# Kernel optimization log

Measured on AMD Instinct MI355X. Metric: run time of the kernel, lower is better.

Reference implementation:

```python
import jax, jax.numpy as jnp
import numpy as np

B, F, T, EPT, S, E, H, LVL = 16384, 512, 4, 2, 2, 256, 128, 2

def _ple_level(xs_task, x_sh, w_task, b_task, w_sh, b_sh, w_gate, b_gate, w_gsh=None, b_gsh=None):
    # xs_task: [T,B,I] per-task inputs; x_sh: [B,I] shared input
    task_out = jax.nn.relu(jnp.einsum('tbi,teio->tbeo', xs_task, w_task) + b_task[:, None])  # [T,B,EPT,E]
    sh_out = jax.nn.relu(jnp.einsum('bi,sio->bso', x_sh, w_sh) + b_sh)                       # [B,S,E]
    t = task_out.shape[0]
    experts = jnp.concatenate([task_out, jnp.broadcast_to(sh_out[None], (t,) + sh_out.shape)], axis=2)  # [T,B,EPT+S,E]
    gate = jax.nn.softmax(jnp.einsum('tbi,tig->tbg', xs_task, w_gate) + b_gate[:, None], axis=-1)
    task_next = jnp.einsum('tbg,tbge->tbe', gate, experts)  # [T,B,E]
    sh_next = None
    if w_gsh is not None:
        # all experts ordered task0_exp0, task0_exp1, task1_exp0, ..., then shared
        bsz = x_sh.shape[0]
        all_exp = jnp.concatenate([jnp.transpose(task_out, (1, 0, 2, 3)).reshape(bsz, -1, task_out.shape[-1]), sh_out], axis=1)
        gsh = jax.nn.softmax(x_sh @ w_gsh + b_gsh, axis=-1)
        sh_next = jnp.einsum('bg,bge->be', gsh, all_exp)
    return task_next, sh_next

def setup_inputs() -> dict:
    key = jax.random.key(0)
    ks = jax.random.split(key, 16)
    sc = 0.02
    d = {
        'x': jax.random.normal(ks[0], (B, F), jnp.float32),
        # level 0 (in_dim=F, has shared gate)
        'w_task0': jax.random.normal(ks[1], (T, EPT, F, E), jnp.float32) * sc,
        'b_task0': jnp.zeros((T, EPT, E), jnp.float32),
        'w_sh0': jax.random.normal(ks[2], (S, F, E), jnp.float32) * sc,
        'b_sh0': jnp.zeros((S, E), jnp.float32),
        'w_gate0': jax.random.normal(ks[3], (T, F, EPT + S), jnp.float32) * sc,
        'b_gate0': jnp.zeros((T, EPT + S), jnp.float32),
        'w_gsh0': jax.random.normal(ks[4], (F, T * EPT + S), jnp.float32) * sc,
        'b_gsh0': jnp.zeros((T * EPT + S,), jnp.float32),
        # level 1 (last; in_dim=E, no shared gate)
        'w_task1': jax.random.normal(ks[5], (T, EPT, E, E), jnp.float32) * sc,
        'b_task1': jnp.zeros((T, EPT, E), jnp.float32),
        'w_sh1': jax.random.normal(ks[6], (S, E, E), jnp.float32) * sc,
        'b_sh1': jnp.zeros((S, E), jnp.float32),
        'w_gate1': jax.random.normal(ks[7], (T, E, EPT + S), jnp.float32) * sc,
        'b_gate1': jnp.zeros((T, EPT + S), jnp.float32),
        # towers
        'w_tw': jax.random.normal(ks[8], (T, E, H), jnp.float32) * sc,
        'b_tw': jnp.zeros((T, H), jnp.float32),
        'w_out': jax.random.normal(ks[9], (T, H, 2), jnp.float32) * sc,
        'b_out': jnp.zeros((T, 2), jnp.float32),
    }
    return d

def reference(x, w_task0, b_task0, w_sh0, b_sh0, w_gate0, b_gate0, w_gsh0, b_gsh0,
              w_task1, b_task1, w_sh1, b_sh1, w_gate1, b_gate1,
              w_tw, b_tw, w_out, b_out):
    xs_task = jnp.broadcast_to(x[None], (T,) + x.shape)  # all tasks see same input at level 0
    t1, sh1 = _ple_level(xs_task, x, w_task0, b_task0, w_sh0, b_sh0, w_gate0, b_gate0, w_gsh0, b_gsh0)
    t2, _ = _ple_level(t1, sh1, w_task1, b_task1, w_sh1, b_sh1, w_gate1, b_gate1)
    h = jax.nn.relu(jnp.einsum('tbe,teh->tbh', t2, w_tw) + b_tw[:, None])
    logits = jnp.einsum('tbh,tho->tbo', h, w_out) + b_out[:, None]
    p = jax.nn.softmax(logits, axis=-1)
    return jnp.clip(p, 1e-15, 1.0 - 1e-15)  # [T,B,2]
```

## Files before the change

### kernel.cpp

```cpp
#include <hip/hip_runtime.h>

typedef unsigned short u16;
typedef __bf16 bf16x8 __attribute__((ext_vector_type(8)));
typedef float f32x4 __attribute__((ext_vector_type(4)));
typedef u16 u16x8 __attribute__((ext_vector_type(8)));

#define B_ 16384

__device__ __forceinline__ u16 f2b(float f){
  unsigned u = __builtin_bit_cast(unsigned, f);
  u = (u + 0x7FFFu + ((u >> 16) & 1u)) >> 16;
  return (u16)u;
}
__device__ __forceinline__ float b2f(u16 v){
  return __builtin_bit_cast(float, ((unsigned)v) << 16);
}
__device__ __forceinline__ void ld8(const u16* __restrict__ p, float* f){
  u16x8 v = *(const u16x8*)p;
  #pragma unroll
  for (int j = 0; j < 8; ++j) f[j] = b2f(v[j]);
}
__device__ __forceinline__ void st8(u16* __restrict__ p, const float* f){
  u16x8 v;
  #pragma unroll
  for (int j = 0; j < 8; ++j) v[j] = f2b(f[j]);
  *(u16x8*)p = v;
}

__device__ __forceinline__ void gload16(const u16* g, u16* lds){
  __builtin_amdgcn_global_load_lds(
      (const __attribute__((address_space(1))) unsigned int*)g,
      (__attribute__((address_space(3))) unsigned int*)lds, 16, 0, 0);
}

__device__ __forceinline__ void core32(const u16* __restrict__ A,
                                       const u16* __restrict__ Wt,
                                       int K, int m0, int n0, int nt,
                                       u16* sm, f32x4 acc[4][4])
{
  const int tid = threadIdx.x, lane = tid & 63, wave = tid >> 6;
  const int wm = ((tid >> 7) & 3) * 64;
  const int wn = ((tid >> 6) & 1) * 64;

  #pragma unroll
  for (int m = 0; m < 4; ++m)
    #pragma unroll
    for (int n = 0; n < 4; ++n) acc[m][n] = (f32x4){0.f, 0.f, 0.f, 0.f};

  const int s_    = (lane & 7) ^ ((lane >> 3) & 7);
  const int srow2 = 2 * (lane >> 3) + (s_ >> 2);
  const int sk    = (s_ & 3) * 8;
  const u16* gsrc[3];
  int gdst[3];
  #pragma unroll
  for (int i = 0; i < 3; ++i) {
    int c = wave * 3 + i;
    if (c < 16) {
      gsrc[i] = A + (size_t)(m0 + c * 16 + srow2) * K + sk;
      gdst[i] = c * 512;
    } else {
      gsrc[i] = Wt + (size_t)(n0 + (c - 16) * 16 + srow2) * K + sk;
      gdst[i] = 8192 + (c - 16) * 512;
    }
  }

  int aoff[4], boff[4];
  #pragma unroll
  for (int m = 0; m < 4; ++m) {
    int r = wm + m * 16 + (lane & 15);
    int L = r >> 1;
    int phys = (((r & 1) << 2) + (lane >> 4)) ^ (L & 7);
    aoff[m] = L * 64 + phys * 8;
  }
  #pragma unroll
  for (int n = 0; n < 4; ++n) {
    int r = wn + n * 16 + (lane & 15);
    int L = r >> 1;
    int phys = (((r & 1) << 2) + (lane >> 4)) ^ (L & 7);
    boff[n] = 8192 + L * 64 + phys * 8;
  }

  #pragma unroll
  for (int j = 0; j < 2; ++j) {
    u16* sl = sm + j * 12288;
    #pragma unroll
    for (int i = 0; i < 3; ++i) gload16(gsrc[i] + j * 32, sl + gdst[i]);
  }
  asm volatile("s_waitcnt vmcnt(3)" ::: "memory");
  __builtin_amdgcn_s_barrier();

  int cs = 0;
  for (int j = 0; j < nt; ++j) {
    if (j + 2 < nt) {
      int ns = cs + 2; ns = (ns >= 3) ? ns - 3 : ns;
      u16* sl = sm + ns * 12288;
      #pragma unroll
      for (int i = 0; i < 3; ++i) gload16(gsrc[i] + (size_t)(j + 2) * 32, sl + gdst[i]);
    }
    const u16* sa = sm + cs * 12288;
    bf16x8 av[4], bv[4];
    #pragma unroll
    for (int m = 0; m < 4; ++m) av[m] = *(const bf16x8*)(sa + aoff[m]);
    #pragma unroll
    for (int n = 0; n < 4; ++n) bv[n] = *(const bf16x8*)(sa + boff[n]);
    __builtin_amdgcn_s_setprio(1);
    #pragma unroll
    for (int m = 0; m < 4; ++m)
      #pragma unroll
      for (int n = 0; n < 4; ++n)
        acc[m][n] = __builtin_amdgcn_mfma_f32_16x16x32_bf16(av[m], bv[n], acc[m][n], 0, 0, 0);
    __builtin_amdgcn_s_setprio(0);
    if (j + 2 < nt)      asm volatile("s_waitcnt vmcnt(3)" ::: "memory");
    else if (j + 1 < nt) asm volatile("s_waitcnt vmcnt(0)" ::: "memory");
    __builtin_amdgcn_s_barrier();
    cs = (cs == 2) ? 0 : cs + 1;
  }
}


__global__ __launch_bounds__(512) void k_gemm0(const u16* __restrict__ xb,
    const u16* __restrict__ Wt0, const float* __restrict__ bias0,
    u16* __restrict__ E0, float* __restrict__ G0L)
{
  __shared__ __align__(16) u16 sm[36864];
  f32x4 acc[4][4];
  const int bid = blockIdx.x;
  const int swz = (bid & 7) * 168 + (bid >> 3);
  const int m0 = (swz / 21) * 256, n0 = (swz % 21) * 128;
  core32(xb, Wt0, 512, m0, n0, 16, sm, acc);
  const int lane = threadIdx.x & 63;
  const int wm = ((threadIdx.x >> 7) & 3) * 64, wn = ((threadIdx.x >> 6) & 1) * 64;
  #pragma unroll
  for (int mi = 0; mi < 4; ++mi)
    #pragma unroll
    for (int ni = 0; ni < 4; ++ni) {
      int gcol = n0 + wn + ni * 16 + (lane & 15);
      float bias = bias0[gcol];
      #pragma unroll
      for (int q = 0; q < 4; ++q) {
        int grow = m0 + wm + mi * 16 + ((lane >> 4) << 2) + q;
        float v = acc[mi][ni][q] + bias;
        if (gcol < 2560)      E0[(size_t)grow * 2560 + gcol] = f2b(fmaxf(v, 0.f));
        else if (gcol < 2586) G0L[(size_t)grow * 26 + (gcol - 2560)] = v;
      }
    }
}

__global__ __launch_bounds__(256) void k_mix0(const u16* __restrict__ E0,
    const float* __restrict__ G0L, const float* __restrict__ WG1T,
    const float* __restrict__ b_gate1, u16* __restrict__ T1SH,
    float* __restrict__ G1S)
{
  const int b = blockIdx.x * 8 + (threadIdx.x >> 5);
  const int e0 = (threadIdx.x & 31) * 8;
  const float* gl = G0L + (size_t)b * 26;
  float g[4][4];
  #pragma unroll
  for (int t = 0; t < 4; ++t) {
    float l0 = gl[t*4+0], l1 = gl[t*4+1], l2 = gl[t*4+2], l3 = gl[t*4+3];
    float m = fmaxf(fmaxf(l0, l1), fmaxf(l2, l3));
    float e0e = expf(l0-m), e1 = expf(l1-m), e2 = expf(l2-m), e3 = expf(l3-m);
    float inv = 1.f / (e0e + e1 + e2 + e3);
    g[t][0] = e0e*inv; g[t][1] = e1*inv; g[t][2] = e2*inv; g[t][3] = e3*inv;
  }
  float gs[10];
  {
    float m = gl[16];
    #pragma unroll
    for (int j = 1; j < 10; ++j) m = fmaxf(m, gl[16 + j]);
    float s = 0.f;
    #pragma unroll
    for (int j = 0; j < 10; ++j) { gs[j] = expf(gl[16 + j] - m); s += gs[j]; }
    float inv = 1.f / s;
    #pragma unroll
    for (int j = 0; j < 10; ++j) gs[j] *= inv;
  }
  const u16* row = E0 + (size_t)b * 2560;
  float sh0[8], sh1[8], shacc[8];
  ld8(row + 2048 + e0, sh0);
  ld8(row + 2304 + e0, sh1);
  #pragma unroll
  for (int j = 0; j < 8; ++j) shacc[j] = gs[8]*sh0[j] + gs[9]*sh1[j];
  float gp[16];
  #pragma unroll
  for (int t = 0; t < 4; ++t) {
    float te0[8], te1[8], v[8];
    ld8(row + (t*2+0)*256 + e0, te0);
    ld8(row + (t*2+1)*256 + e0, te1);
    #pragma unroll
    for (int j = 0; j < 8; ++j) {
      v[j] = g[t][0]*te0[j] + g[t][1]*te1[j] + g[t][2]*sh0[j] + g[t][3]*sh1[j];
      shacc[j] += gs[t*2+0]*te0[j] + gs[t*2+1]*te1[j];
    }
    st8(T1SH + ((size_t)t * B_ + b) * 256 + e0, v);
    #pragma unroll
    for (int gg = 0; gg < 4; ++gg) {
      const float* wv = WG1T + ((size_t)(t * 4 + gg) * 256 + e0);
      float s = 0.f;
      #pragma unroll
      for (int j = 0; j < 8; ++j) s += v[j] * wv[j];
      gp[t * 4 + gg] = s;
    }
  }
  st8(T1SH + ((size_t)4 * B_ + b) * 256 + e0, shacc);
  #pragma unroll
  for (int i = 0; i < 16; ++i) {
    #pragma unroll
    for (int off = 1; off < 32; off <<= 1)
      gp[i] += __shfl_xor(gp[i], off, 32);
  }
  if ((threadIdx.x & 31) == 0) {
    float* orow = G1S + (size_t)b * 16;
    #pragma unroll
    for (int z = 0; z < 4; ++z) {
      float l0 = gp[z*4+0] + b_gate1[z*4+0];
      float l1 = gp[z*4+1] + b_gate1[z*4+1];
      float l2 = gp[z*4+2] + b_gate1[z*4+2];
      float l3 = gp[z*4+3] + b_gate1[z*4+3];
      float m = fmaxf(fmaxf(l0, l1), fmaxf(l2, l3));
      float x0 = expf(l0-m), x1 = expf(l1-m), x2 = expf(l2-m), x3 = expf(l3-m);
      float inv = 1.f / (x0 + x1 + x2 + x3);
      orow[z*4+0] = x0*inv; orow[z*4+1] = x1*inv;
      orow[z*4+2] = x2*inv; orow[z*4+3] = x3*inv;
    }
  }
}

__global__ __launch_bounds__(512) void k_gemm1(const u16* __restrict__ T1SH,
    const u16* __restrict__ Wt1, const float* __restrict__ bias1,
    u16* __restrict__ E1, u16* __restrict__ SH1E)
{
  __shared__ __align__(16) u16 sm[36864];
  f32x4 acc[4][4];
  const int bid = blockIdx.x;
  const int swz = (bid & 7) * 160 + (bid >> 3);
  const int mi_ = swz / 20, pan = swz % 20;
  const int z  = pan >> 2;
  const int n0 = (pan & 3) * 128;
  const int m0 = mi_ * 256;
  core32(T1SH + (size_t)z * B_ * 256, Wt1 + (size_t)z * 512 * 256, 256, m0, n0, 8, sm, acc);
  const int lane = threadIdx.x & 63;
  const int wm = ((threadIdx.x >> 7) & 3) * 64, wn = ((threadIdx.x >> 6) & 1) * 64;
  const float* bias = bias1 + z * 512;
  #pragma unroll
  for (int mi = 0; mi < 4; ++mi)
    #pragma unroll
    for (int ni = 0; ni < 4; ++ni) {
      int gcol = n0 + wn + ni * 16 + (lane & 15);
      float bv = bias[gcol];
      #pragma unroll
      for (int q = 0; q < 4; ++q) {
        int grow = m0 + wm + mi * 16 + ((lane >> 4) << 2) + q;
        float v = fmaxf(acc[mi][ni][q] + bv, 0.f);
        if (z < 4) E1[((size_t)z * B_ + grow) * 512 + gcol] = f2b(v);
        else       SH1E[(size_t)grow * 512 + gcol] = f2b(v);
      }
    }
}

__global__ __launch_bounds__(256) void k_tower2(const u16* __restrict__ E1,
    const u16* __restrict__ SH1E, const float* __restrict__ G1S,
    const u16* __restrict__ Wtw, const float* __restrict__ b_tw,
    const float* __restrict__ w_out, const float* __restrict__ b_out,
    float* __restrict__ out)
{
  __shared__ __align__(16) u16 sm[32768];
  __shared__ float part[2][128][2];
  f32x4 acc[4][4];
  const int z = blockIdx.z;
  const int m0 = blockIdx.x * 128;
  const int tid = threadIdx.x, lane = tid & 63, wave = tid >> 6;
  const int wm = ((tid >> 7) & 1) * 64, wn = ((tid >> 6) & 1) * 64;

  #pragma unroll
  for (int mi = 0; mi < 4; ++mi)
    #pragma unroll
    for (int ni = 0; ni < 4; ++ni) acc[mi][ni] = (f32x4){0.f, 0.f, 0.f, 0.f};

  const int srow  = lane >> 3;
  const int gslot = (lane & 7) ^ srow;
  const int koff0 = gslot * 8;

  int growA[4], adst[4], bdst[4];
  const u16* bsrc[4];
  #pragma unroll
  for (int i = 0; i < 4; ++i) {
    int c = wave * 4 + i;
    growA[i] = m0 + c * 8 + srow;
    adst[i]  = c * 512;
    bsrc[i]  = Wtw + (size_t)z * 128 * 256 + (size_t)(c * 8 + srow) * 256 + koff0;
    bdst[i]  = 8192 + c * 512;
  }
  const u16* E1z = E1 + (size_t)z * B_ * 512;

  int aoff[2][4], boff[2][4];
  #pragma unroll
  for (int kk = 0; kk < 2; ++kk) {
    #pragma unroll
    for (int m = 0; m < 4; ++m) {
      int r = wm + m * 16 + (lane & 15);
      aoff[kk][m] = r * 64 + (((kk * 4 + (lane >> 4)) ^ (r & 7)) * 8);
    }
    #pragma unroll
    for (int n = 0; n < 4; ++n) {
      int r = wn + n * 16 + (lane & 15);
      boff[kk][n] = 8192 + r * 64 + (((kk * 4 + (lane >> 4)) ^ (r & 7)) * 8);
    }
  }

  #define STAGE_T(J, BUF) do {                                                 \
    u16* buf_ = (BUF);                                                         \
    _Pragma("unroll")                                                          \
    for (int i_ = 0; i_ < 4; ++i_) {                                           \
      size_t eoff_ = (size_t)growA[i_] * 512 + (J) * 64 + koff0;               \
      u16x8 ea_ = *(const u16x8*)(E1z + eoff_);                                \
      u16x8 eb_ = *(const u16x8*)(E1z + eoff_ + 256);                          \
      u16x8 sa_ = *(const u16x8*)(SH1E + eoff_);                               \
      u16x8 sb_ = *(const u16x8*)(SH1E + eoff_ + 256);                         \
      float4 g_ = *(const float4*)(G1S + (size_t)growA[i_] * 16 + z * 4);      \
      u16x8 o_;                                                                \
      _Pragma("unroll")                                                        \
      for (int jj_ = 0; jj_ < 8; ++jj_)                                        \
        o_[jj_] = f2b(g_.x * b2f(ea_[jj_]) + g_.y * b2f(eb_[jj_])              \
                    + g_.z * b2f(sa_[jj_]) + g_.w * b2f(sb_[jj_]));            \
      *(uint4*)(buf_ + adst[i_] + lane * 8) = __builtin_bit_cast(uint4, o_);   \
      gload16(bsrc[i_] + (J) * 64, buf_ + bdst[i_]);                           \
    }                                                                          \
  } while (0)

  STAGE_T(0, sm);
  __syncthreads();

  #pragma unroll
  for (int t = 0; t < 4; ++t) {
    if (t + 1 < 4) STAGE_T(t + 1, sm + ((t + 1) & 1) * 16384);
    const u16* sa = sm + (t & 1) * 16384;
    #pragma unroll
    for (int kk = 0; kk < 2; ++kk) {
      bf16x8 av[4], bv[4];
      #pragma unroll
      for (int m = 0; m < 4; ++m) av[m] = *(const bf16x8*)(sa + aoff[kk][m]);
      #pragma unroll
      for (int n = 0; n < 4; ++n) bv[n] = *(const bf16x8*)(sa + boff[kk][n]);
      #pragma unroll
      for (int m = 0; m < 4; ++m)
        #pragma unroll
        for (int n = 0; n < 4; ++n)
          acc[m][n] = __builtin_amdgcn_mfma_f32_16x16x32_bf16(av[m], bv[n], acc[m][n], 0, 0, 0);
    }
    if (t + 1 < 4) __syncthreads();
  }
  #undef STAGE_T

  #pragma unroll
  for (int mi = 0; mi < 4; ++mi) {
    #pragma unroll
    for (int r = 0; r < 4; ++r) {
      float p0 = 0.f, p1 = 0.f;
      #pragma unroll
      for (int ni = 0; ni < 4; ++ni) {
        int col = wn + ni * 16 + (lane & 15);
        float h = fmaxf(acc[mi][ni][r] + b_tw[z * 128 + col], 0.f);
        p0 += h * w_out[(z * 128 + col) * 2 + 0];
        p1 += h * w_out[(z * 128 + col) * 2 + 1];
      }
      #pragma unroll
      for (int off = 1; off < 16; off <<= 1) {
        p0 += __shfl_xor(p0, off);
        p1 += __shfl_xor(p1, off);
      }
      if ((lane & 15) == 0) {
        int rowl = wm + mi * 16 + ((lane >> 4) << 2) + r;
        part[wn >> 6][rowl][0] = p0;
        part[wn >> 6][rowl][1] = p1;
      }
    }
  }
  __syncthreads();
  if (threadIdx.x < 128) {
    int rowl = threadIdx.x;
    float l0 = part[0][rowl][0] + part[1][rowl][0] + b_out[z * 2 + 0];
    float l1 = part[0][rowl][1] + part[1][rowl][1] + b_out[z * 2 + 1];
    float mx = fmaxf(l0, l1);
    float e0 = expf(l0 - mx), e1 = expf(l1 - mx);
    float inv = 1.f / (e0 + e1);
    float p0 = fminf(fmaxf(e0 * inv, 1e-15f), 1.0f);
    float p1 = fminf(fmaxf(e1 * inv, 1e-15f), 1.0f);
    size_t o = ((size_t)z * B_ + m0 + rowl) * 2;
    out[o] = p0; out[o + 1] = p1;
  }
}

__global__ void k_prep(const float* __restrict__ x,
    const float* __restrict__ w_task0, const float* __restrict__ b_task0,
    const float* __restrict__ w_sh0,   const float* __restrict__ b_sh0,
    const float* __restrict__ w_gate0, const float* __restrict__ b_gate0,
    const float* __restrict__ w_gsh0,  const float* __restrict__ b_gsh0,
    const float* __restrict__ w_task1, const float* __restrict__ b_task1,
    const float* __restrict__ w_sh1,   const float* __restrict__ b_sh1,
    const float* __restrict__ w_gate1, const float* __restrict__ w_tw,
    u16* __restrict__ xb, u16* __restrict__ Wt0, float* __restrict__ bias0,
    u16* __restrict__ Wt1, float* __restrict__ bias1, u16* __restrict__ Wtw,
    float* __restrict__ WG1T)
{
  size_t i = (size_t)blockIdx.x * 256 + threadIdx.x;
  const size_t S_X8  = (size_t)16384 * 512 / 8;
  const size_t S_WT0 = (size_t)2816 * 512;
  const size_t S_B0  = 2816;
  const size_t S_WT1 = (size_t)5 * 512 * 256;
  const size_t S_B1  = 5 * 512;
  const size_t S_WTW = (size_t)4 * 128 * 256;
  const size_t S_WG1 = 4096;

  if (i < S_X8) {
    size_t o = i * 8;
    float4 a = *(const float4*)(x + o);
    float4 b = *(const float4*)(x + o + 4);
    u16x8 v;
    v[0] = f2b(a.x); v[1] = f2b(a.y); v[2] = f2b(a.z); v[3] = f2b(a.w);
    v[4] = f2b(b.x); v[5] = f2b(b.y); v[6] = f2b(b.z); v[7] = f2b(b.w);
    *(u16x8*)(xb + o) = v;
    return;
  }
  i -= S_X8;
  if (i < S_WT0) {
    int c = (int)(i / 512), f = (int)(i % 512);
    float v = 0.f;
    if (c < 2048)      { int te = c >> 8, o = c & 255; v = w_task0[((size_t)te * 512 + f) * 256 + o]; }
    else if (c < 2560) { int s = (c - 2048) >> 8, o = c & 255; v = w_sh0[((size_t)s * 512 + f) * 256 + o]; }
    else if (c < 2576) { int q = c - 2560; int t = q >> 2, gg = q & 3; v = w_gate0[((size_t)t * 512 + f) * 4 + gg]; }
    else if (c < 2586) { int j = c - 2576; v = w_gsh0[(size_t)f * 10 + j]; }
    Wt0[i] = f2b(v);
    return;
  }
  i -= S_WT0;
  if (i < S_B0) {
    int c = (int)i; float v = 0.f;
    if (c < 2048)      { int te = c >> 8, o = c & 255; v = b_task0[te * 256 + o]; }
    else if (c < 2560) { int s = (c - 2048) >> 8, o = c & 255; v = b_sh0[s * 256 + o]; }
    else if (c < 2576) { v = b_gate0[c - 2560]; }
    else if (c < 2586) { v = b_gsh0[c - 2576]; }
    bias0[c] = v;
    return;
  }
  i -= S_B0;
  if (i < S_WT1) {
    int z = (int)(i / (512 * 256)); int rem = (int)(i % (512 * 256));
    int c = rem / 256, f = rem % 256;
    float v;
    if (z < 4) { int ee = c >> 8, o = c & 255; v = w_task1[(((size_t)(z * 2 + ee)) * 256 + f) * 256 + o]; }
    else       { int s = c >> 8, o = c & 255; v = w_sh1[((size_t)s * 256 + f) * 256 + o]; }
    Wt1[i] = f2b(v);
    return;
  }
  i -= S_WT1;
  if (i < S_B1) {
    int z = (int)(i / 512); int c = (int)(i % 512);
    float v;
    if (z < 4) { int ee = c >> 8, o = c & 255; v = b_task1[(z * 2 + ee) * 256 + o]; }
    else       { int s = c >> 8, o = c & 255; v = b_sh1[s * 256 + o]; }
    bias1[(size_t)z * 512 + c] = v;
    return;
  }
  i -= S_B1;
  if (i < S_WTW) {
    int z = (int)(i / (128 * 256)); int rem = (int)(i % (128 * 256));
    int h = rem / 256, f = rem % 256;
    Wtw[i] = f2b(w_tw[((size_t)z * 256 + f) * 128 + h]);
    return;
  }
  i -= S_WTW;
  if (i < S_WG1) {
    int t = (int)(i >> 10), gg = (int)((i >> 8) & 3), e = (int)(i & 255);
    WG1T[i] = w_gate1[((size_t)t * 256 + e) * 4 + gg];
    return;
  }
}

extern "C" void kernel_launch(void* const* d_in, const int* in_sizes, int n_in,
                              void* d_out, int out_size, void* d_ws, size_t ws_size,
                              hipStream_t stream)
{
  (void)in_sizes; (void)n_in; (void)out_size; (void)ws_size;
  const float* x       = (const float*)d_in[0];
  const float* w_task0 = (const float*)d_in[1];
  const float* b_task0 = (const float*)d_in[2];
  const float* w_sh0   = (const float*)d_in[3];
  const float* b_sh0   = (const float*)d_in[4];
  const float* w_gate0 = (const float*)d_in[5];
  const float* b_gate0 = (const float*)d_in[6];
  const float* w_gsh0  = (const float*)d_in[7];
  const float* b_gsh0  = (const float*)d_in[8];
  const float* w_task1 = (const float*)d_in[9];
  const float* b_task1 = (const float*)d_in[10];
  const float* w_sh1   = (const float*)d_in[11];
  const float* b_sh1   = (const float*)d_in[12];
  const float* w_gate1 = (const float*)d_in[13];
  const float* b_gate1 = (const float*)d_in[14];
  const float* w_tw    = (const float*)d_in[15];
  const float* b_tw    = (const float*)d_in[16];
  const float* w_out   = (const float*)d_in[17];
  const float* b_out   = (const float*)d_in[18];
  float* out = (float*)d_out;

  char* ws = (char*)d_ws;
  u16*   XB    = (u16*)  (ws + 0);
  u16*   SH1E  = (u16*)  (ws + 0);
  u16*   WT0   = (u16*)  (ws + 16777216);
  float* BIAS0 = (float*)(ws + 19660800);
  u16*   WT1   = (u16*)  (ws + 19672064);
  float* BIAS1 = (float*)(ws + 20982784);
  u16*   WTW   = (u16*)  (ws + 20993024);
  u16*   E0    = (u16*)  (ws + 21255168);
  float* G0L   = (float*)(ws + 105141248);
  u16*   T1SH  = (u16*)  (ws + 106845184);
  u16*   E1    = (u16*)  (ws + 148788224);
  float* G1S   = (float*)(ws + 215897088);
  float* WG1T  = (float*)(ws + 216945664);

  k_prep<<<12837, 256, 0, stream>>>(x, w_task0, b_task0, w_sh0, b_sh0, w_gate0, b_gate0,
      w_gsh0, b_gsh0, w_task1, b_task1, w_sh1, b_sh1, w_gate1, w_tw,
      XB, WT0, BIAS0, WT1, BIAS1, WTW, WG1T);
  k_gemm0<<<1344, 512, 0, stream>>>(XB, WT0, BIAS0, E0, G0L);
  k_mix0<<<2048, 256, 0, stream>>>(E0, G0L, WG1T, b_gate1, T1SH, G1S);
  k_gemm1<<<1280, 512, 0, stream>>>(T1SH, WT1, BIAS1, E1, SH1E);
  k_tower2<<<dim3(128, 1, 4), 256, 0, stream>>>(E1, SH1E, G1S, WTW, b_tw, w_out, b_out, out);
}
```

Baseline: 172.0 us.

## Fuse level-0 expert gating into task GEMM epilogue, split gate and shared GEMMs

Level 0 is split into three kernels. A small kernel computes the gate logits and softmaxes. A GEMM produces the shared experts. A task-expert GEMM, whose weights are interleaved so that each 128-column tile holds all 8 task experts for 16 output features, applies the gated mixing in its epilogue through LDS and writes T1SH directly. This removes the large E0 intermediate (B×2560 bf16) round trip and the separate mix pass, at the cost of extra kernel launches, a serial gate kernel that uses wave reductions, and scattered 2-byte SH0E reads in the epilogue.

```diff
diff --git a/kernel.cpp b/kernel.cpp
--- a/kernel.cpp
+++ b/kernel.cpp
@@ -4,6 +4,7 @@
 typedef __bf16 bf16x8 __attribute__((ext_vector_type(8)));
 typedef float f32x4 __attribute__((ext_vector_type(4)));
 typedef u16 u16x8 __attribute__((ext_vector_type(8)));
+typedef u16 u16x4 __attribute__((ext_vector_type(4)));
 
 #define B_ 16384
 
@@ -118,16 +119,72 @@
 }
 
 
-__global__ __launch_bounds__(512) void k_gemm0(const u16* __restrict__ xb,
-    const u16* __restrict__ Wt0, const float* __restrict__ bias0,
-    u16* __restrict__ E0, float* __restrict__ G0L)
+__global__ __launch_bounds__(256) void k_gate0(const u16* __restrict__ xb,
+    const u16* __restrict__ WG0T, const float* __restrict__ b_gate0,
+    const float* __restrict__ b_gsh0, float* __restrict__ G0S)
+{
+  const int lane = threadIdx.x & 63, wave = threadIdx.x >> 6;
+  const int rbase = blockIdx.x * 64 + wave * 16;
+  u16x8 w[26];
+  #pragma unroll
+  for (int g = 0; g < 26; ++g)
+    w[g] = *(const u16x8*)(WG0T + (size_t)g * 512 + lane * 8);
+  float bias[26];
+  #pragma unroll
+  for (int g = 0; g < 26; ++g) bias[g] = (g < 16) ? b_gate0[g] : b_gsh0[g - 16];
+
+  for (int it = 0; it < 16; ++it) {
+    int row = rbase + it;
+    float f[8]; ld8(xb + (size_t)row * 512 + lane * 8, f);
+    float lg[26];
+    #pragma unroll
+    for (int g = 0; g < 26; ++g) {
+      float p = 0.f;
+      #pragma unroll
+      for (int j = 0; j < 8; ++j) p += f[j] * b2f(w[g][j]);
+      #pragma unroll
+      for (int off = 1; off < 64; off <<= 1) p += __shfl_xor(p, off);
+      lg[g] = p + bias[g];
+    }
+    float tg[16];
+    #pragma unroll
+    for (int t = 0; t < 4; ++t) {
+      float m = fmaxf(fmaxf(lg[4*t], lg[4*t+1]), fmaxf(lg[4*t+2], lg[4*t+3]));
+      float e0 = expf(lg[4*t]-m), e1 = expf(lg[4*t+1]-m);
+      float e2 = expf(lg[4*t+2]-m), e3 = expf(lg[4*t+3]-m);
+      float inv = 1.f / (e0+e1+e2+e3);
+      tg[4*t] = e0*inv; tg[4*t+1] = e1*inv; tg[4*t+2] = e2*inv; tg[4*t+3] = e3*inv;
+    }
+    float sg[10];
+    {
+      float m = lg[16];
+      #pragma unroll
+      for (int j = 1; j < 10; ++j) m = fmaxf(m, lg[16+j]);
+      float ssum = 0.f;
+      #pragma unroll
+      for (int j = 0; j < 10; ++j) { sg[j] = expf(lg[16+j]-m); ssum += sg[j]; }
+      float inv = 1.f / ssum;
+      #pragma unroll
+      for (int j = 0; j < 10; ++j) sg[j] *= inv;
+    }
+    float* orow = G0S + (size_t)row * 32;
+    #pragma unroll
+    for (int g = 0; g < 16; ++g) if (lane == g) orow[g] = tg[g];
+    #pragma unroll
+    for (int j = 0; j < 10; ++j) if (lane == 16 + j) orow[16 + j] = sg[j];
+  }
+}
+
+__global__ __launch_bounds__(512) void k_gemm0sh(const u16* __restrict__ xb,
+    const u16* __restrict__ WT0S, const float* __restrict__ bias0s,
+    u16* __restrict__ SH0E)
 {
   __shared__ __align__(16) u16 sm[36864];
   f32x4 acc[4][4];
   const int bid = blockIdx.x;
-  const int swz = (bid & 7) * 168 + (bid >> 3);
-  const int m0 = (swz / 21) * 256, n0 = (swz % 21) * 128;
-  core32(xb, Wt0, 512, m0, n0, 16, sm, acc);
+  const int swz = (bid & 7) * 32 + (bid >> 3);
+  const int m0 = (swz >> 2) * 256, n0 = (swz & 3) * 128;
+  core32(xb, WT0S, 512, m0, n0, 16, sm, acc);
   const int lane = threadIdx.x & 63;
   const int wm = ((threadIdx.x >> 7) & 3) * 64, wn = ((threadIdx.x >> 6) & 1) * 64;
   #pragma unroll
@@ -135,64 +192,92 @@
     #pragma unroll
     for (int ni = 0; ni < 4; ++ni) {
       int gcol = n0 + wn + ni * 16 + (lane & 15);
-      float bias = bias0[gcol];
+      float bias = bias0s[gcol];
       #pragma unroll
       for (int q = 0; q < 4; ++q) {
         int grow = m0 + wm + mi * 16 + ((lane >> 4) << 2) + q;
-        float v = acc[mi][ni][q] + bias;
-        if (gcol < 2560)      E0[(size_t)grow * 2560 + gcol] = f2b(fmaxf(v, 0.f));
-        else if (gcol < 2586) G0L[(size_t)grow * 26 + (gcol - 2560)] = v;
+        SH0E[(size_t)grow * 512 + gcol] = f2b(fmaxf(acc[mi][ni][q] + bias, 0.f));
       }
     }
 }
 
-__global__ __launch_bounds__(256) void k_mix0(const u16* __restrict__ E0,
-    const float* __restrict__ G0L, const float* __restrict__ WG1T,
-    const float* __restrict__ b_gate1, u16* __restrict__ T1SH,
+__global__ __launch_bounds__(512) void k_gemm0t(const u16* __restrict__ xb,
+    const u16* __restrict__ WT0T, const float* __restrict__ bias0t,
+    const u16* __restrict__ SH0E, const float* __restrict__ G0S,
+    u16* __restrict__ T1SH)
+{
+  __shared__ __align__(16) u16 sm[36864];
+  f32x4 acc[4][4];
+  const int bid = blockIdx.x;
+  const int swz = (bid & 7) * 128 + (bid >> 3);
+  const int m0 = (swz >> 4) * 256, n0 = (swz & 15) * 128;
+  core32(xb, WT0T, 512, m0, n0, 16, sm, acc);
+
+  const int tid = threadIdx.x, lane = tid & 63;
+  const int wmIdx = (tid >> 7) & 3;
+  const int wn = ((tid >> 6) & 1) * 64;
+  float* lds2 = (float*)sm;
+  const int ebase = n0 >> 3;
+
+  for (int pair = 0; pair < 2; ++pair) {
+    __syncthreads();
+    #pragma unroll
+    for (int mi2 = 0; mi2 < 2; ++mi2) {
+      int mi = pair * 2 + mi2;
+      #pragma unroll
+      for (int ni = 0; ni < 4; ++ni) {
+        int colL = wn + ni * 16 + (lane & 15);
+        float bias = bias0t[n0 + colL];
+        int el = colL >> 3, s2 = colL & 7;
+        #pragma unroll
+        for (int q = 0; q < 4; ++q) {
+          int rl = wmIdx * 32 + mi2 * 16 + ((lane >> 4) << 2) + q;
+          lds2[rl * 136 + el * 9 + s2] = fmaxf(acc[mi][ni][q] + bias, 0.f);
+        }
+      }
+    }
+    __syncthreads();
+    const int r = tid >> 2, p = tid & 3;
+    const int grow = m0 + (r >> 5) * 64 + pair * 32 + (r & 31);
+    const float* gp = G0S + (size_t)grow * 32;
+    u16x4 o[5];
+    #pragma unroll
+    for (int k = 0; k < 4; ++k) {
+      int el = p * 4 + k;
+      float ex[8];
+      #pragma unroll
+      for (int s2 = 0; s2 < 8; ++s2) ex[s2] = lds2[r * 136 + el * 9 + s2];
+      int eg = ebase + el;
+      float sh0v = b2f(SH0E[(size_t)grow * 512 + eg]);
+      float sh1v = b2f(SH0E[(size_t)grow * 512 + 256 + eg]);
+      float sha = gp[24] * sh0v + gp[25] * sh1v;
+      #pragma unroll
+      for (int t = 0; t < 4; ++t) {
+        float v = gp[t*4+0] * ex[2*t] + gp[t*4+1] * ex[2*t+1]
+                + gp[t*4+2] * sh0v    + gp[t*4+3] * sh1v;
+        o[t][k] = f2b(v);
+        sha += gp[16 + 2*t] * ex[2*t] + gp[17 + 2*t] * ex[2*t+1];
+      }
+      o[4][k] = f2b(sha);
+    }
+    int eg0 = ebase + p * 4;
+    #pragma unroll
+    for (int t = 0; t < 5; ++t)
+      *(u16x4*)(T1SH + ((size_t)t * B_ + grow) * 256 + eg0) = o[t];
+  }
+}
+
+__global__ __launch_bounds__(256) void k_gate1(const u16* __restrict__ T1SH,
+    const float* __restrict__ WG1T, const float* __restrict__ b_gate1,
     float* __restrict__ G1S)
 {
   const int b = blockIdx.x * 8 + (threadIdx.x >> 5);
   const int e0 = (threadIdx.x & 31) * 8;
-  const float* gl = G0L + (size_t)b * 26;
-  float g[4][4];
+  float gp[16];
   #pragma unroll
   for (int t = 0; t < 4; ++t) {
-    float l0 = gl[t*4+0], l1 = gl[t*4+1], l2 = gl[t*4+2], l3 = gl[t*4+3];
-    float m = fmaxf(fmaxf(l0, l1), fmaxf(l2, l3));
-    float e0e = expf(l0-m), e1 = expf(l1-m), e2 = expf(l2-m), e3 = expf(l3-m);
-    float inv = 1.f / (e0e + e1 + e2 + e3);
-    g[t][0] = e0e*inv; g[t][1] = e1*inv; g[t][2] = e2*inv; g[t][3] = e3*inv;
-  }
-  float gs[10];
-  {
-    float m = gl[16];
-    #pragma unroll
-    for (int j = 1; j < 10; ++j) m = fmaxf(m, gl[16 + j]);
-    float s = 0.f;
-    #pragma unroll
-    for (int j = 0; j < 10; ++j) { gs[j] = expf(gl[16 + j] - m); s += gs[j]; }
-    float inv = 1.f / s;
-    #pragma unroll
-    for (int j = 0; j < 10; ++j) gs[j] *= inv;
-  }
-  const u16* row = E0 + (size_t)b * 2560;
-  float sh0[8], sh1[8], shacc[8];
-  ld8(row + 2048 + e0, sh0);
-  ld8(row + 2304 + e0, sh1);
-  #pragma unroll
-  for (int j = 0; j < 8; ++j) shacc[j] = gs[8]*sh0[j] + gs[9]*sh1[j];
-  float gp[16];
-  #pragma unroll
-  for (int t = 0; t < 4; ++t) {
-    float te0[8], te1[8], v[8];
-    ld8(row + (t*2+0)*256 + e0, te0);
-    ld8(row + (t*2+1)*256 + e0, te1);
-    #pragma unroll
-    for (int j = 0; j < 8; ++j) {
-      v[j] = g[t][0]*te0[j] + g[t][1]*te1[j] + g[t][2]*sh0[j] + g[t][3]*sh1[j];
-      shacc[j] += gs[t*2+0]*te0[j] + gs[t*2+1]*te1[j];
-    }
-    st8(T1SH + ((size_t)t * B_ + b) * 256 + e0, v);
+    float v[8];
+    ld8(T1SH + ((size_t)t * B_ + b) * 256 + e0, v);
     #pragma unroll
     for (int gg = 0; gg < 4; ++gg) {
       const float* wv = WG1T + ((size_t)(t * 4 + gg) * 256 + e0);
@@ -202,7 +287,6 @@
       gp[t * 4 + gg] = s;
     }
   }
-  st8(T1SH + ((size_t)4 * B_ + b) * 256 + e0, shacc);
   #pragma unroll
   for (int i = 0; i < 16; ++i) {
     #pragma unroll
@@ -394,19 +478,22 @@
 __global__ void k_prep(const float* __restrict__ x,
     const float* __restrict__ w_task0, const float* __restrict__ b_task0,
     const float* __restrict__ w_sh0,   const float* __restrict__ b_sh0,
-    const float* __restrict__ w_gate0, const float* __restrict__ b_gate0,
-    const float* __restrict__ w_gsh0,  const float* __restrict__ b_gsh0,
+    const float* __restrict__ w_gate0, const float* __restrict__ w_gsh0,
     const float* __restrict__ w_task1, const float* __restrict__ b_task1,
     const float* __restrict__ w_sh1,   const float* __restrict__ b_sh1,
     const float* __restrict__ w_gate1, const float* __restrict__ w_tw,
-    u16* __restrict__ xb, u16* __restrict__ Wt0, float* __restrict__ bias0,
-    u16* __restrict__ Wt1, float* __restrict__ bias1, u16* __restrict__ Wtw,
-    float* __restrict__ WG1T)
+    u16* __restrict__ xb, u16* __restrict__ WT0T, float* __restrict__ bias0t,
+    u16* __restrict__ WT0S, float* __restrict__ bias0s,
+    u16* __restrict__ WG0T, u16* __restrict__ Wt1, float* __restrict__ bias1,
+    u16* __restrict__ Wtw, float* __restrict__ WG1T)
 {
   size_t i = (size_t)blockIdx.x * 256 + threadIdx.x;
   const size_t S_X8  = (size_t)16384 * 512 / 8;
-  const size_t S_WT0 = (size_t)2816 * 512;
-  const size_t S_B0  = 2816;
+  const size_t S_T   = (size_t)2048 * 512;
+  const size_t S_BT  = 2048;
+  const size_t S_S   = (size_t)512 * 512;
+  const size_t S_BS  = 512;
+  const size_t S_WG0 = 26 * 512;
   const size_t S_WT1 = (size_t)5 * 512 * 256;
   const size_t S_B1  = 5 * 512;
   const size_t S_WTW = (size_t)4 * 128 * 256;
@@ -423,27 +510,41 @@
     return;
   }
   i -= S_X8;
-  if (i < S_WT0) {
+  if (i < S_T) {
     int c = (int)(i / 512), f = (int)(i % 512);
-    float v = 0.f;
-    if (c < 2048)      { int te = c >> 8, o = c & 255; v = w_task0[((size_t)te * 512 + f) * 256 + o]; }
-    else if (c < 2560) { int s = (c - 2048) >> 8, o = c & 255; v = w_sh0[((size_t)s * 512 + f) * 256 + o]; }
-    else if (c < 2576) { int q = c - 2560; int t = q >> 2, gg = q & 3; v = w_gate0[((size_t)t * 512 + f) * 4 + gg]; }
-    else if (c < 2586) { int j = c - 2576; v = w_gsh0[(size_t)f * 10 + j]; }
-    Wt0[i] = f2b(v);
-    return;
-  }
-  i -= S_WT0;
-  if (i < S_B0) {
-    int c = (int)i; float v = 0.f;
-    if (c < 2048)      { int te = c >> 8, o = c & 255; v = b_task0[te * 256 + o]; }
-    else if (c < 2560) { int s = (c - 2048) >> 8, o = c & 255; v = b_sh0[s * 256 + o]; }
-    else if (c < 2576) { v = b_gate0[c - 2560]; }
-    else if (c < 2586) { v = b_gsh0[c - 2576]; }
-    bias0[c] = v;
-    return;
-  }
-  i -= S_B0;
+    int te = c & 7, e = c >> 3;
+    WT0T[i] = f2b(w_task0[((size_t)te * 512 + f) * 256 + e]);
+    return;
+  }
+  i -= S_T;
+  if (i < S_BT) {
+    int te = (int)i & 7, e = (int)i >> 3;
+    bias0t[i] = b_task0[te * 256 + e];
+    return;
+  }
+  i -= S_BT;
+  if (i < S_S) {
+    int c = (int)(i / 512), f = (int)(i % 512);
+    int s = c >> 8, e = c & 255;
+    WT0S[i] = f2b(w_sh0[((size_t)s * 512 + f) * 256 + e]);
+    return;
+  }
+  i -= S_S;
+  if (i < S_BS) {
+    int s = (int)i >> 8, e = (int)i & 255;
+    bias0s[i] = b_sh0[s * 256 + e];
+    return;
+  }
+  i -= S_BS;
+  if (i < S_WG0) {
+    int g = (int)(i / 512), f = (int)(i % 512);
+    float v;
+    if (g < 16) { int t = g >> 2, gg = g & 3; v = w_gate0[((size_t)t * 512 + f) * 4 + gg]; }
+    else        { v = w_gsh0[(size_t)f * 10 + (g - 16)]; }
+    WG0T[i] = f2b(v);
+    return;
+  }
+  i -= S_WG0;
   if (i < S_WT1) {
     int z = (int)(i / (512 * 256)); int rem = (int)(i % (512 * 256));
     int c = rem / 256, f = rem % 256;
@@ -506,23 +607,28 @@
   char* ws = (char*)d_ws;
   u16*   XB    = (u16*)  (ws + 0);
   u16*   SH1E  = (u16*)  (ws + 0);
-  u16*   WT0   = (u16*)  (ws + 16777216);
-  float* BIAS0 = (float*)(ws + 19660800);
-  u16*   WT1   = (u16*)  (ws + 19672064);
-  float* BIAS1 = (float*)(ws + 20982784);
-  u16*   WTW   = (u16*)  (ws + 20993024);
-  u16*   E0    = (u16*)  (ws + 21255168);
-  float* G0L   = (float*)(ws + 105141248);
-  u16*   T1SH  = (u16*)  (ws + 106845184);
-  u16*   E1    = (u16*)  (ws + 148788224);
-  float* G1S   = (float*)(ws + 215897088);
-  float* WG1T  = (float*)(ws + 216945664);
-
-  k_prep<<<12837, 256, 0, stream>>>(x, w_task0, b_task0, w_sh0, b_sh0, w_gate0, b_gate0,
-      w_gsh0, b_gsh0, w_task1, b_task1, w_sh1, b_sh1, w_gate1, w_tw,
-      XB, WT0, BIAS0, WT1, BIAS1, WTW, WG1T);
-  k_gemm0<<<1344, 512, 0, stream>>>(XB, WT0, BIAS0, E0, G0L);
-  k_mix0<<<2048, 256, 0, stream>>>(E0, G0L, WG1T, b_gate1, T1SH, G1S);
+  u16*   WT0T  = (u16*)  (ws + 16777216);
+  float* BIAS0T= (float*)(ws + 18874368);
+  u16*   WT0S  = (u16*)  (ws + 18882560);
+  float* BIAS0S= (float*)(ws + 19406848);
+  u16*   WG0T  = (u16*)  (ws + 19408896);
+  u16*   WT1   = (u16*)  (ws + 19435520);
+  float* BIAS1 = (float*)(ws + 20746240);
+  u16*   WTW   = (u16*)  (ws + 20756480);
+  float* WG1T  = (float*)(ws + 21018624);
+  u16*   SH0E  = (u16*)  (ws + 21035008);
+  float* G0S   = (float*)(ws + 37812224);
+  u16*   T1SH  = (u16*)  (ws + 39909376);
+  u16*   E1    = (u16*)  (ws + 81852416);
+  float* G1S   = (float*)(ws + 148961280);
+
+  k_prep<<<12376, 256, 0, stream>>>(x, w_task0, b_task0, w_sh0, b_sh0,
+      w_gate0, w_gsh0, w_task1, b_task1, w_sh1, b_sh1, w_gate1, w_tw,
+      XB, WT0T, BIAS0T, WT0S, BIAS0S, WG0T, WT1, BIAS1, WTW, WG1T);
+  k_gate0<<<256, 256, 0, stream>>>(XB, WG0T, b_gate0, b_gsh0, G0S);
+  k_gemm0sh<<<256, 512, 0, stream>>>(XB, WT0S, BIAS0S, SH0E);
+  k_gemm0t<<<1024, 512, 0, stream>>>(XB, WT0T, BIAS0T, SH0E, G0S, T1SH);
+  k_gate1<<<2048, 256, 0, stream>>>(T1SH, WG1T, b_gate1, G1S);
   k_gemm1<<<1280, 512, 0, stream>>>(T1SH, WT1, BIAS1, E1, SH1E);
   k_tower2<<<dim3(128, 1, 4), 256, 0, stream>>>(E1, SH1E, G1S, WTW, b_tw, w_out, b_out, out);
 }
```

New measurement: 248.5 us. 1.44x slower.
